# Kernel optimization log

Measured on AMD Instinct MI355X. Metric: run time of the kernel, lower is better.

## Reference

```python
import jax, jax.numpy as jnp
import numpy as np

B, T, D, H = 8, 1024, 1024, 16
HD = D // H  # 64
FF = 4 * D


def setup_inputs() -> dict:
    key = jax.random.key(0)
    ks = jax.random.split(key, 16)
    s = lambda k, shape, scale: (jax.random.normal(k, shape, dtype=jnp.float32) * scale)
    return {
        "x": s(ks[0], (B, T, D), 1.0),
        "ln1_g": jnp.ones((D,), jnp.float32),
        "ln1_b": jnp.zeros((D,), jnp.float32),
        "ln2_g": jnp.ones((D,), jnp.float32),
        "ln2_b": jnp.zeros((D,), jnp.float32),
        "Wq": s(ks[1], (H, D, HD), 0.02), "bq": jnp.zeros((H, HD), jnp.float32),
        "Wk": s(ks[2], (H, D, HD), 0.02), "bk": jnp.zeros((H, HD), jnp.float32),
        "Wv": s(ks[3], (H, D, HD), 0.02), "bv": jnp.zeros((H, HD), jnp.float32),
        "Wo": s(ks[4], (D, D), 0.02), "bo": jnp.zeros((D,), jnp.float32),
        "W1": s(ks[5], (D, FF), 0.02), "b1": jnp.zeros((FF,), jnp.float32),
        "W2": s(ks[6], (FF, D), 0.02), "b2": jnp.zeros((D,), jnp.float32),
    }


def layer_norm(x, g, b, eps=1e-5):
    mu = jnp.mean(x, axis=-1, keepdims=True)
    var = jnp.mean(jnp.square(x - mu), axis=-1, keepdims=True)
    return (x - mu) * jax.lax.rsqrt(var + eps) * g + b


def reference(x, ln1_g, ln1_b, ln2_g, ln2_b, Wq, bq, Wk, bk, Wv, bv, Wo, bo, W1, b1, W2, b2):
    h = layer_norm(x, ln1_g, ln1_b)
    # Per-head Q/K/V projections, batched over heads (equivalent to the
    # Python loop of per-head Linears in the original module).
    q = jnp.einsum("btd,hde->bhte", h, Wq) + bq[None, :, None, :]
    k = jnp.einsum("btd,hde->bhte", h, Wk) + bk[None, :, None, :]
    v = jnp.einsum("btd,hde->bhte", h, Wv) + bv[None, :, None, :]
    scores = jnp.einsum("bhte,bhse->bhts", q, k) / jnp.sqrt(jnp.float32(HD))
    att = jax.nn.softmax(scores, axis=-1)  # no causal mask in source
    ctx = jnp.einsum("bhts,bhse->bhte", att, v)
    # concat heads along feature dim
    ctx = jnp.transpose(ctx, (0, 2, 1, 3)).reshape(B, T, D)
    attn_out = ctx @ Wo + bo
    x = x + attn_out
    h2 = layer_norm(x, ln2_g, ln2_b)
    ff = jax.nn.gelu(h2 @ W1 + b1, approximate=False) @ W2 + b2
    return x + ff
```

## Files before the change

kernel.cpp:

```cpp
#include <hip/hip_runtime.h>
#include <hip/hip_bf16.h>
#include <cstdint>
#include <cstddef>


typedef __bf16 bf16;
typedef __bf16 bf16x8 __attribute__((ext_vector_type(8)));
typedef __bf16 bf16x4 __attribute__((ext_vector_type(4)));
typedef float  f32x4  __attribute__((ext_vector_type(4)));
typedef uint32_t u32x4 __attribute__((ext_vector_type(4)));

#define BB    8
#define TT    1024
#define DD    1024
#define HH    16
#define HDIM  64
#define FFD   4096
#define MROWS (BB*TT)

__device__ __forceinline__ void async_ld16(const void* g, void* l) {
  __builtin_amdgcn_global_load_lds(
      (const __attribute__((address_space(1))) uint32_t*)g,
      (__attribute__((address_space(3))) uint32_t*)l, 16, 0, 0);
}

__device__ __forceinline__ float gelu_f(float v) {
  float z = 0.7978845608028654f * (v + 0.044715f * v * v * v);
  z = fminf(fmaxf(z, -9.0f), 9.0f);
  const float e = __expf(-2.0f * z);
  const float th = 1.0f - __fdividef(2.0f * e, 1.0f + e);
  return 0.5f * v * (1.0f + th);
}

__device__ __forceinline__ float exp2_fast(float x) {
  float r; asm("v_exp_f32 %0, %1" : "=v"(r) : "v"(x)); return r;
}
__device__ __forceinline__ uint32_t cvt_pk_bf16(float a, float b) {
  uint32_t r; asm("v_cvt_pk_bf16_f32 %0, %1, %2" : "=v"(r) : "v"(a), "v"(b));
  return r;
}

__global__ void k_transpose_cast(const float* __restrict__ src, bf16* __restrict__ dst,
                                 int K, int N) {
  __shared__ float tile[32][33];
  const size_t boff = (size_t)blockIdx.z * K * N;
  src += boff; dst += boff;
  const int k0 = blockIdx.y * 32, n0 = blockIdx.x * 32;
  const int tx = threadIdx.x, ty = threadIdx.y;
#pragma unroll
  for (int i = 0; i < 4; ++i)
    tile[ty + i*8][tx] = src[(size_t)(k0 + ty + i*8) * N + n0 + tx];
  __syncthreads();
#pragma unroll
  for (int i = 0; i < 4; ++i)
    dst[(size_t)(n0 + ty + i*8) * K + k0 + tx] = (bf16)tile[tx][ty + i*8];
}

__global__ void k_concat_bias(const float* __restrict__ bq, const float* __restrict__ bk,
                              const float* __restrict__ bv, float* __restrict__ out) {
  int i = blockIdx.x * 256 + threadIdx.x;
  float v = (i < 1024) ? bq[i] : (i < 2048) ? bk[i - 1024] : bv[i - 2048];
  out[i] = v;
}

__global__ void k_transpose_v(const bf16* __restrict__ qkv, bf16* __restrict__ vT) {
  __shared__ bf16 tile[32][33];
  const int bh = blockIdx.z;
  const int b = bh >> 4, h = bh & 15;
  const int t0 = blockIdx.x * 32, e0 = blockIdx.y * 32;
  const int tx = threadIdx.x, ty = threadIdx.y;
  const bf16* src = qkv + (size_t)b * TT * 3072 + 2048 + h * 64;
#pragma unroll
  for (int i = 0; i < 4; ++i)
    tile[ty + i*8][tx] = src[(size_t)(t0 + ty + i*8) * 3072 + e0 + tx];
  __syncthreads();
  bf16* dst = vT + ((size_t)bh * 64 + e0) * TT + t0;
#pragma unroll
  for (int i = 0; i < 4; ++i)
    dst[(size_t)(ty + i*8) * TT + tx] = tile[tx][ty + i*8];
}

__global__ void k_layernorm(const float* __restrict__ x, const float* __restrict__ g,
                            const float* __restrict__ b, bf16* __restrict__ out) {
  const int row = blockIdx.x, tid = threadIdx.x;
  const float* xr = x + (size_t)row * DD;
  f32x4 v = *(const f32x4*)(xr + tid * 4);
  float s  = v[0] + v[1] + v[2] + v[3];
  float ss = v[0]*v[0] + v[1]*v[1] + v[2]*v[2] + v[3]*v[3];
#pragma unroll
  for (int m = 1; m < 64; m <<= 1) { s += __shfl_xor(s, m); ss += __shfl_xor(ss, m); }
  __shared__ float red[8];
  const int wid = tid >> 6;
  if ((tid & 63) == 0) { red[wid*2] = s; red[wid*2+1] = ss; }
  __syncthreads();
  s  = red[0] + red[2] + red[4] + red[6];
  ss = red[1] + red[3] + red[5] + red[7];
  const float mu = s * (1.0f / DD);
  const float var = ss * (1.0f / DD) - mu * mu;
  const float rs = rsqrtf(var + 1e-5f);
  bf16x4 o;
#pragma unroll
  for (int j = 0; j < 4; ++j)
    o[j] = (bf16)((v[j] - mu) * rs * g[tid*4 + j] + b[tid*4 + j]);
  *(bf16x4*)&out[(size_t)row * DD + tid * 4] = o;
}

#define RD_B(reg, base) { _Pragma("unroll") \
    for (int nf = 0; nf < 4; ++nf) reg[nf] = *(const bf16x8*)((base) + nf*1024); }
#define RD_A4(reg, base, mb) { _Pragma("unroll") \
    for (int mf = 0; mf < 4; ++mf) reg[mf] = *(const bf16x8*)((base) + (mb+mf)*1024); }
#define MM(areg, breg, mb) { _Pragma("unroll") \
    for (int mf = 0; mf < 4; ++mf) _Pragma("unroll") \
      for (int nf = 0; nf < 4; ++nf) \
        acc[mb+mf][nf] = __builtin_amdgcn_mfma_f32_16x16x32_bf16(areg[mf], breg[nf], acc[mb+mf][nf], 0, 0, 0); }
#define SGA(off, lb) { async_ld16(aG0 + (off), (lb)+0*64);   async_ld16(aG1 + (off), (lb)+64*64); \
                       async_ld16(aG2 + (off), (lb)+128*64); async_ld16(aG3 + (off), (lb)+192*64); }
#define SGB(off, lb) { async_ld16(bG0 + (off), (lb)+0*64);   async_ld16(bG1 + (off), (lb)+64*64); \
                       async_ld16(bG2 + (off), (lb)+128*64); async_ld16(bG3 + (off), (lb)+192*64); }
#define SGB2a(off, lb) { async_ld16(bG0 + (off), (lb)+0*64);   async_ld16(bG1 + (off), (lb)+64*64); }
#define SGB2b(off, lb) { async_ld16(bG2 + (off), (lb)+128*64); async_ld16(bG3 + (off), (lb)+192*64); }
#define WAIT_LGKM { asm volatile("s_waitcnt lgkmcnt(0)" ::: "memory"); __builtin_amdgcn_sched_barrier(0); }
#define VMC(n)  { asm volatile("s_waitcnt vmcnt(" #n ")" ::: "memory"); __builtin_amdgcn_sched_barrier(0); }
#define BAR __builtin_amdgcn_s_barrier()
#define PR1 __builtin_amdgcn_s_setprio(1)
#define PR0 __builtin_amdgcn_s_setprio(0)

#define GEMM256_PREAMBLE \
  __shared__ __align__(16) bf16 As[2][256 * 64]; \
  __shared__ __align__(16) bf16 Bs[2][256 * 64]; \
  const int tid = threadIdx.x; \
  const int w = tid >> 6, l = tid & 63; \
  const int wm = w >> 2, wn = w & 3; \
  const int l15 = l & 15, l4 = l >> 4; \
  const int nbx = N >> 8; \
  const int nwg = gridDim.x; \
  const int cpx = nwg >> 3; \
  const int swz = (blockIdx.x & 7) * cpx + (blockIdx.x >> 3); \
  const int m0 = (swz / nbx) << 8, n0 = (swz % nbx) << 8; \
  f32x4 acc[8][4] = {}; \
  const int l7 = l15 & 7; \
  const int c0 = (l4 ^ l7) * 8; \
  const int c1 = ((4 + l4) ^ l7) * 8; \
  const bf16* const A00 = &As[0][(wm*128 + l15)*64 + c0]; \
  const bf16* const A01 = &As[0][(wm*128 + l15)*64 + c1]; \
  const bf16* const A10 = &As[1][(wm*128 + l15)*64 + c0]; \
  const bf16* const A11 = &As[1][(wm*128 + l15)*64 + c1]; \
  const bf16* const B00 = &Bs[0][(wn*64 + l15)*64 + c0]; \
  const bf16* const B01 = &Bs[0][(wn*64 + l15)*64 + c1]; \
  const bf16* const B10 = &Bs[1][(wn*64 + l15)*64 + c0]; \
  const bf16* const B11 = &Bs[1][(wn*64 + l15)*64 + c1]; \
  const int srow = l >> 3, sch = l & 7; \
  const int schx = (sch ^ srow) * 8; \
  const bf16* const aG0 = A  + (size_t)(m0 + w*8 + srow) * K + schx; \
  const bf16* const aG1 = aG0 + (size_t)64 * K; \
  const bf16* const aG2 = aG0 + (size_t)128 * K; \
  const bf16* const aG3 = aG0 + (size_t)192 * K; \
  const bf16* const bG0 = Bt + (size_t)(n0 + w*8 + srow) * K + schx; \
  const bf16* const bG1 = bG0 + (size_t)64 * K; \
  const bf16* const bG2 = bG0 + (size_t)128 * K; \
  const bf16* const bG3 = bG0 + (size_t)192 * K; \
  bf16* const LA0 = (bf16*)As[0] + w*512; \
  bf16* const LA1 = (bf16*)As[1] + w*512; \
  bf16* const LB0 = (bf16*)Bs[0] + w*512; \
  bf16* const LB1 = (bf16*)Bs[1] + w*512; \
  const int NT = K >> 6;

#define GEMM256_EPILOGUE \
  _Pragma("unroll") \
  for (int mf = 0; mf < 8; ++mf) { \
    _Pragma("unroll") \
    for (int r = 0; r < 4; ++r) { \
      const size_t grow = (size_t)(m0 + wm*128 + mf*16 + l4*4 + r); \
      const size_t rowoff = grow * (size_t)N; \
      _Pragma("unroll") \
      for (int nf = 0; nf < 4; ++nf) { \
        const int gcol = n0 + wn*64 + nf*16 + l15; \
        float v = acc[mf][nf][r] + bias[gcol]; \
        if constexpr (MODE == 1) v = gelu_f(v); \
        outb[rowoff + gcol] = (bf16)v; \
      } \
    } \
  }

template<int MODE>
__global__ __launch_bounds__(512, 2)
void k_gemm256(const bf16* __restrict__ A, const bf16* __restrict__ Bt,
               const float* __restrict__ bias, bf16* __restrict__ outb,
               int M, int N, int K) {
  GEMM256_PREAMBLE

  SGA(0, LA0)  SGB2a(0, LB0) SGB2b(0, LB0)  SGA(64, LA1)
  VMC(4);
  BAR;

  size_t ko = 0;
  for (int T = 0; T < NT; T += 2) {
    const bool nl  = (T + 2 < NT);
    const bool nl2 = (T + 3 < NT);
    bf16x8 b0[4], b1[4], alo[4], ahi[4];

    RD_B(b0, B00) RD_A4(alo, A00, 0)
    SGB2a(ko + 64, LB1)
    BAR; WAIT_LGKM;
    PR1; MM(alo, b0, 0) PR0;
    BAR;
    RD_A4(ahi, A00, 4)
    SGB2b(ko + 64, LB1)
    BAR; WAIT_LGKM;
    PR1; MM(ahi, b0, 4) PR0;
    BAR;
    RD_B(b1, B01) RD_A4(alo, A01, 0) RD_A4(ahi, A01, 4)
    BAR; WAIT_LGKM;
    PR1; MM(alo, b1, 0) PR0;
    BAR;
    if (nl) SGA(ko + 128, LA0)
    PR1; MM(ahi, b1, 4) PR0;
    if (nl) { VMC(4); } else { VMC(0); }
    BAR;

    RD_B(b0, B10) RD_A4(alo, A10, 0)
    if (nl) SGB2a(ko + 128, LB0)
    BAR; WAIT_LGKM;
    PR1; MM(alo, b0, 0) PR0;
    BAR;
    RD_A4(ahi, A10, 4)
    if (nl) SGB2b(ko + 128, LB0)
    BAR; WAIT_LGKM;
    PR1; MM(ahi, b0, 4) PR0;
    BAR;
    RD_B(b1, B11) RD_A4(alo, A11, 0) RD_A4(ahi, A11, 4)
    BAR; WAIT_LGKM;
    PR1; MM(alo, b1, 0) PR0;
    BAR;
    if (nl2) SGA(ko + 192, LA1)
    PR1; MM(ahi, b1, 4) PR0;
    if (nl2) { VMC(4); } else { VMC(0); }
    BAR;

    ko += 128;
  }

  GEMM256_EPILOGUE
}

template<int MODE>
__global__ __launch_bounds__(512, 2)
void k_gemm256b(const bf16* __restrict__ A, const bf16* __restrict__ Bt,
                const float* __restrict__ bias, bf16* __restrict__ outb,
                int M, int N, int K) {
  GEMM256_PREAMBLE

  SGA(0, LA0)  SGB(0, LB0)  SGA(64, LA1)  SGB(64, LB1)
  VMC(8);
  BAR;

  size_t ko = 0;
  for (int T = 0; T < NT; T += 2) {
    const bool nl  = (T + 2 < NT);
    const bool nl2 = (T + 3 < NT);
    bf16x8 b0[4], b1[4], alo[4], ahi[4];

    RD_B(b0, B00) RD_A4(alo, A00, 0)
    BAR; WAIT_LGKM;
    PR1; MM(alo, b0, 0) PR0;
    BAR;
    RD_A4(ahi, A00, 4)
    BAR; WAIT_LGKM;
    PR1; MM(ahi, b0, 4) PR0;
    BAR;
    RD_B(b1, B01) RD_A4(alo, A01, 0) RD_A4(ahi, A01, 4)
    BAR; WAIT_LGKM;
    PR1; MM(alo, b1, 0) PR0;
    BAR;
    if (nl) { SGA(ko + 128, LA0) SGB(ko + 128, LB0) }
    PR1; MM(ahi, b1, 4) PR0;
    if (nl) { VMC(8); } else { VMC(0); }
    BAR;

    RD_B(b0, B10) RD_A4(alo, A10, 0)
    BAR; WAIT_LGKM;
    PR1; MM(alo, b0, 0) PR0;
    BAR;
    RD_A4(ahi, A10, 4)
    BAR; WAIT_LGKM;
    PR1; MM(ahi, b0, 4) PR0;
    BAR;
    RD_B(b1, B11) RD_A4(alo, A11, 0) RD_A4(ahi, A11, 4)
    BAR; WAIT_LGKM;
    PR1; MM(alo, b1, 0) PR0;
    BAR;
    if (nl2) { SGA(ko + 192, LA1) SGB(ko + 192, LB1) }
    PR1; MM(ahi, b1, 4) PR0;
    if (nl2) { VMC(8); } else { VMC(0); }
    BAR;

    ko += 128;
  }

  GEMM256_EPILOGUE
}

template<int MODE>
__global__ __launch_bounds__(256)
void k_gemm(const bf16* __restrict__ A, const bf16* __restrict__ Bt,
            const float* __restrict__ bias, const float* __restrict__ res,
            bf16* __restrict__ outb, float* __restrict__ outf,
            int M, int N, int K) {
  __shared__ __align__(16) bf16 As[128 * 64];
  __shared__ __align__(16) bf16 Bs[128 * 64];
  const int tid = threadIdx.x;
  const int w = tid >> 6, l = tid & 63;
  const int wm = w >> 1, wn = w & 1;
  const int l15 = l & 15, l4 = l >> 4;
  const int m0 = blockIdx.y * 128, n0 = blockIdx.x * 128;

  f32x4 acc[4][4] = {};

  const int l7 = l15 & 7;
  const int c0 = (l4 ^ l7) * 8, c1 = ((4 + l4) ^ l7) * 8;
  const bf16* const Ab = &As[(wm*64 + l15)*64];
  const bf16* const Bb = &Bs[(wn*64 + l15)*64];

  const int sr8 = l >> 3, sl7 = l & 7;
  const int schx = (sl7 ^ sr8) * 8;
  const bf16* const gA0 = A  + (size_t)(m0 + w*32 + sr8) * K + schx;
  const bf16* const gA1 = gA0 + (size_t)8 * K;
  const bf16* const gA2 = gA0 + (size_t)16 * K;
  const bf16* const gA3 = gA0 + (size_t)24 * K;
  const bf16* const gB0 = Bt + (size_t)(n0 + w*32 + sr8) * K + schx;
  const bf16* const gB1 = gB0 + (size_t)8 * K;
  const bf16* const gB2 = gB0 + (size_t)16 * K;
  const bf16* const gB3 = gB0 + (size_t)24 * K;
  bf16* const lA = (bf16*)As + w*32*64;
  bf16* const lB = (bf16*)Bs + w*32*64;

  for (int k0 = 0; k0 < K; k0 += 64) {
    async_ld16(gA0 + k0, lA);          async_ld16(gA1 + k0, lA + 8*64);
    async_ld16(gA2 + k0, lA + 16*64);  async_ld16(gA3 + k0, lA + 24*64);
    async_ld16(gB0 + k0, lB);          async_ld16(gB1 + k0, lB + 8*64);
    async_ld16(gB2 + k0, lB + 16*64);  async_ld16(gB3 + k0, lB + 24*64);
    __syncthreads();
#pragma unroll
    for (int kk = 0; kk < 2; ++kk) {
      const int cc = kk ? c1 : c0;
      bf16x8 af[4], bfr[4];
#pragma unroll
      for (int mf = 0; mf < 4; ++mf) af[mf] = *(const bf16x8*)(Ab + mf*1024 + cc);
#pragma unroll
      for (int nf = 0; nf < 4; ++nf) bfr[nf] = *(const bf16x8*)(Bb + nf*1024 + cc);
#pragma unroll
      for (int mf = 0; mf < 4; ++mf)
#pragma unroll
        for (int nf = 0; nf < 4; ++nf)
          acc[mf][nf] = __builtin_amdgcn_mfma_f32_16x16x32_bf16(af[mf], bfr[nf], acc[mf][nf], 0, 0, 0);
    }
    __syncthreads();
  }

#pragma unroll
  for (int mf = 0; mf < 4; ++mf) {
#pragma unroll
    for (int r = 0; r < 4; ++r) {
      const size_t grow = (size_t)(m0 + wm*64 + mf*16 + l4*4 + r);
      const size_t rowoff = grow * (size_t)N;
#pragma unroll
      for (int nf = 0; nf < 4; ++nf) {
        const int gcol = n0 + wn*64 + nf*16 + l15;
        float v = acc[mf][nf][r] + bias[gcol];
        if constexpr (MODE == 1) v = gelu_f(v);
        if constexpr (MODE == 2) {
          v += res[rowoff + gcol];
          outf[rowoff + gcol] = v;
        } else {
          outb[rowoff + gcol] = (bf16)v;
        }
      }
    }
  }
}

__global__ __launch_bounds__(512)
void k_attn(const bf16* __restrict__ qkv, const bf16* __restrict__ vT,
            bf16* __restrict__ ctx) {
  const int tid = threadIdx.x;
  const int w = tid >> 6, l = tid & 63;
  const int l15 = l & 15, l4 = l >> 4;

  const int gid = ((int)blockIdx.x & 7) * 128 + ((int)blockIdx.x >> 3);
  const int qt = gid & 7;
  const int bh = gid >> 3;
  const int h = bh & 15, b = bh >> 4;

  __shared__ __align__(16) bf16 Ks[2][64 * 64];
  __shared__ __align__(16) bf16 Vs[2][64 * 64];

  const bf16* base = qkv + (size_t)b * TT * 3072;
  const bf16* Qp = base + h * 64;
  const bf16* Kp = base + 1024 + h * 64;
  const bf16* Vtp = vT + (size_t)bh * HDIM * TT;

  const float SCL = 0.125f * 1.44269504f;
  const float THR = 8.0f * 1.44269504f;

  const int qrow = qt * 128 + w * 16 + l15;
  bf16x8 qf[2];
  {
    bf16x8 q0 = *(const bf16x8*)&Qp[(size_t)qrow * 3072 + l4 * 8];
    bf16x8 q1 = *(const bf16x8*)&Qp[(size_t)qrow * 3072 + 32 + l4 * 8];
#pragma unroll
    for (int j = 0; j < 8; ++j) {
      qf[0][j] = (bf16)((float)q0[j] * SCL);
      qf[1][j] = (bf16)((float)q1[j] * SCL);
    }
  }

  f32x4 oacc[4] = {};
  float mrow = -1e30f;
  float lrow = 0.f;

  const int l7 = l15 & 7;
  const int c0 = (l4 ^ l7) * 8, c1 = ((4 + l4) ^ l7) * 8;

  const int aL0 = (((l4 & 1) << 5) + l15) << 2;
  const int aL1 = aL0 + 64;
  const bool hi = (l & 32) != 0;

  const int srow = w * 8 + (l >> 3);
  const int sch = (l & 7) ^ (srow & 7);

  auto stage = [&](int buf, int t) {
    const int kv0 = t * 64;
    async_ld16(Kp + (size_t)(kv0 + srow) * 3072 + sch * 8, &Ks[buf][w * 512]);
    async_ld16(Vtp + (size_t)srow * TT + kv0 + sch * 8, &Vs[buf][w * 512]);
  };

  stage(0, 0);
  for (int t = 0; t < TT / 64; ++t) {
    const int cur = t & 1;
    __syncthreads();
    if (t + 1 < TT / 64) stage(cur ^ 1, t + 1);

    const bf16* const Kc = &Ks[cur][l15 * 64];
    const bf16* const Vc = &Vs[cur][l15 * 64];

    f32x4 sacc[4] = {};
    __builtin_amdgcn_s_setprio(1);
#pragma unroll
    for (int nf = 0; nf < 4; ++nf) {
      bf16x8 k0 = *(const bf16x8*)(Kc + nf*1024 + c0);
      bf16x8 k1 = *(const bf16x8*)(Kc + nf*1024 + c1);
      sacc[nf] = __builtin_amdgcn_mfma_f32_16x16x32_bf16(k0, qf[0], sacc[nf], 0, 0, 0);
      sacc[nf] = __builtin_amdgcn_mfma_f32_16x16x32_bf16(k1, qf[1], sacc[nf], 0, 0, 0);
    }
    __builtin_amdgcn_s_setprio(0);

    float m = fmaxf(fmaxf(sacc[0][0], sacc[0][1]), fmaxf(sacc[0][2], sacc[0][3]));
#pragma unroll
    for (int nf = 1; nf < 4; ++nf)
      m = fmaxf(m, fmaxf(fmaxf(sacc[nf][0], sacc[nf][1]), fmaxf(sacc[nf][2], sacc[nf][3])));
    m = fmaxf(m, __shfl_xor(m, 16));
    m = fmaxf(m, __shfl_xor(m, 32));

    const int ok = (m <= mrow + THR);
    if (!__all(ok)) {
      const float mn = fmaxf(mrow, m);
      const float e = exp2_fast(mrow - mn);
      mrow = mn;
      lrow *= e;
      const int qb = l4 << 2;
      float e0 = __shfl(e, qb + 0), e1 = __shfl(e, qb + 1);
      float e2 = __shfl(e, qb + 2), e3 = __shfl(e, qb + 3);
#pragma unroll
      for (int nf = 0; nf < 4; ++nf) {
        oacc[nf][0] *= e0; oacc[nf][1] *= e1;
        oacc[nf][2] *= e2; oacc[nf][3] *= e3;
      }
    }

    float p[4][4];
    float ls = 0.f;
    uint32_t pk0[4], pk1[4];
#pragma unroll
    for (int nf = 0; nf < 4; ++nf) {
#pragma unroll
      for (int r = 0; r < 4; ++r) {
        p[nf][r] = exp2_fast(sacc[nf][r] - mrow);
        ls += p[nf][r];
      }
      pk0[nf] = cvt_pk_bf16(p[nf][0], p[nf][1]);
      pk1[nf] = cvt_pk_bf16(p[nf][2], p[nf][3]);
    }
    ls += __shfl_xor(ls, 16);
    ls += __shfl_xor(ls, 32);
    lrow += ls;

    __builtin_amdgcn_s_setprio(1);
#pragma unroll
    for (int kk = 0; kk < 2; ++kk) {
      const int nfa = 2*kk, nfb = 2*kk + 1;
      int u0 = __builtin_amdgcn_ds_bpermute(aL0, (int)pk0[nfa]);
      int u1 = __builtin_amdgcn_ds_bpermute(aL0, (int)pk0[nfb]);
      int v0 = __builtin_amdgcn_ds_bpermute(aL0, (int)pk1[nfa]);
      int v1 = __builtin_amdgcn_ds_bpermute(aL0, (int)pk1[nfb]);
      int x0 = __builtin_amdgcn_ds_bpermute(aL1, (int)pk0[nfa]);
      int x1 = __builtin_amdgcn_ds_bpermute(aL1, (int)pk0[nfb]);
      int y0 = __builtin_amdgcn_ds_bpermute(aL1, (int)pk1[nfa]);
      int y1 = __builtin_amdgcn_ds_bpermute(aL1, (int)pk1[nfb]);
      u32x4 pw;
      pw[0] = (uint32_t)(hi ? u1 : u0);
      pw[1] = (uint32_t)(hi ? v1 : v0);
      pw[2] = (uint32_t)(hi ? x1 : x0);
      pw[3] = (uint32_t)(hi ? y1 : y0);
      bf16x8 pa = __builtin_bit_cast(bf16x8, pw);
      const int cc = kk ? c1 : c0;
#pragma unroll
      for (int nf = 0; nf < 4; ++nf) {
        bf16x8 vb = *(const bf16x8*)(Vc + nf*1024 + cc);
        oacc[nf] = __builtin_amdgcn_mfma_f32_16x16x32_bf16(pa, vb, oacc[nf], 0, 0, 0);
      }
    }
    __builtin_amdgcn_s_setprio(0);
  }

  const int qb = l4 << 2;
  float li0 = 1.0f / __shfl(lrow, qb + 0);
  float li1 = 1.0f / __shfl(lrow, qb + 1);
  float li2 = 1.0f / __shfl(lrow, qb + 2);
  float li3 = 1.0f / __shfl(lrow, qb + 3);
  bf16* outp = ctx + ((size_t)b * TT + qt * 128 + w * 16) * DD + h * 64;
#pragma unroll
  for (int nf = 0; nf < 4; ++nf) {
    outp[(size_t)(qb + 0) * DD + l15 + nf*16] = (bf16)(oacc[nf][0] * li0);
    outp[(size_t)(qb + 1) * DD + l15 + nf*16] = (bf16)(oacc[nf][1] * li1);
    outp[(size_t)(qb + 2) * DD + l15 + nf*16] = (bf16)(oacc[nf][2] * li2);
    outp[(size_t)(qb + 3) * DD + l15 + nf*16] = (bf16)(oacc[nf][3] * li3);
  }
}

extern "C" void kernel_launch(void* const* d_in, const int* in_sizes, int n_in,
                              void* d_out, int out_size, void* d_ws, size_t ws_size,
                              hipStream_t stream) {
  const float* x     = (const float*)d_in[0];
  const float* ln1_g = (const float*)d_in[1];
  const float* ln1_b = (const float*)d_in[2];
  const float* ln2_g = (const float*)d_in[3];
  const float* ln2_b = (const float*)d_in[4];
  const float* Wq    = (const float*)d_in[5];
  const float* bq    = (const float*)d_in[6];
  const float* Wk    = (const float*)d_in[7];
  const float* bk    = (const float*)d_in[8];
  const float* Wv    = (const float*)d_in[9];
  const float* bv    = (const float*)d_in[10];
  const float* Wo    = (const float*)d_in[11];
  const float* bo    = (const float*)d_in[12];
  const float* W1    = (const float*)d_in[13];
  const float* b1    = (const float*)d_in[14];
  const float* W2    = (const float*)d_in[15];
  const float* b2    = (const float*)d_in[16];
  float* out = (float*)d_out;

  char* ws = (char*)d_ws;
  bf16* h1    = (bf16*)(ws + 0);
  bf16* vT    = (bf16*)(ws + 0);
  bf16* qkv   = (bf16*)(ws + 16777216);
  bf16* ctx   = (bf16*)(ws + 67108864);
  bf16* u     = (bf16*)(ws + 16777216);
  float* x1   = (float*)(ws + 83886080);
  bf16* wtqkv = (bf16*)(ws + 117440512);
  bf16* wot   = (bf16*)(ws + 123731968);
  bf16* w1t   = (bf16*)(ws + 125829120);
  bf16* w2t   = (bf16*)(ws + 134217728);
  float* bqkv = (float*)(ws + 142606336);
  bf16* h2 = h1;

  dim3 tb(32, 8);
  k_transpose_cast<<<dim3(2, 32, 16), tb, 0, stream>>>(Wq, wtqkv, DD, HDIM);
  k_transpose_cast<<<dim3(2, 32, 16), tb, 0, stream>>>(Wk, wtqkv + 1024*1024, DD, HDIM);
  k_transpose_cast<<<dim3(2, 32, 16), tb, 0, stream>>>(Wv, wtqkv + 2048*1024, DD, HDIM);
  k_transpose_cast<<<dim3(32, 32, 1), tb, 0, stream>>>(Wo, wot, DD, DD);
  k_transpose_cast<<<dim3(128, 32, 1), tb, 0, stream>>>(W1, w1t, DD, FFD);
  k_transpose_cast<<<dim3(32, 128, 1), tb, 0, stream>>>(W2, w2t, FFD, DD);
  k_concat_bias<<<dim3(12), 256, 0, stream>>>(bq, bk, bv, bqkv);

  k_layernorm<<<dim3(MROWS), 256, 0, stream>>>(x, ln1_g, ln1_b, h1);

  k_gemm256<0><<<dim3((MROWS/256)*(3072/256)), 512, 0, stream>>>(
      h1, wtqkv, bqkv, qkv, MROWS, 3072, DD);

  k_transpose_v<<<dim3(32, 2, 128), tb, 0, stream>>>(qkv, vT);

  k_attn<<<dim3(1024), 512, 0, stream>>>(qkv, vT, ctx);

  k_gemm<2><<<dim3(8, 64), 256, 0, stream>>>(ctx, wot, bo, x,
                                             nullptr, x1, MROWS, DD, DD);

  k_layernorm<<<dim3(MROWS), 256, 0, stream>>>(x1, ln2_g, ln2_b, h2);

  k_gemm256b<1><<<dim3((MROWS/256)*(FFD/256)), 512, 0, stream>>>(
      h2, w1t, b1, u, MROWS, FFD, DD);

  k_gemm<2><<<dim3(8, 64), 256, 0, stream>>>(u, w2t, b2, x1,
                                             nullptr, out, MROWS, DD, FFD);

  (void)in_sizes; (void)n_in; (void)out_size; (void)ws_size;
}
```

Measured before the change: 413.7 us.

## Load FF1 GEMM B operand directly from global into registers, skipping LDS

```diff
diff --git a/kernel.cpp b/kernel.cpp
--- a/kernel.cpp
+++ b/kernel.cpp
@@ -117,53 +117,12 @@
                        async_ld16(aG2 + (off), (lb)+128*64); async_ld16(aG3 + (off), (lb)+192*64); }
 #define SGB(off, lb) { async_ld16(bG0 + (off), (lb)+0*64);   async_ld16(bG1 + (off), (lb)+64*64); \
                        async_ld16(bG2 + (off), (lb)+128*64); async_ld16(bG3 + (off), (lb)+192*64); }
-#define SGB2a(off, lb) { async_ld16(bG0 + (off), (lb)+0*64);   async_ld16(bG1 + (off), (lb)+64*64); }
-#define SGB2b(off, lb) { async_ld16(bG2 + (off), (lb)+128*64); async_ld16(bG3 + (off), (lb)+192*64); }
 #define WAIT_LGKM { asm volatile("s_waitcnt lgkmcnt(0)" ::: "memory"); __builtin_amdgcn_sched_barrier(0); }
+#define LGKM4 { asm volatile("s_waitcnt lgkmcnt(4)" ::: "memory"); __builtin_amdgcn_sched_barrier(0); }
 #define VMC(n)  { asm volatile("s_waitcnt vmcnt(" #n ")" ::: "memory"); __builtin_amdgcn_sched_barrier(0); }
 #define BAR __builtin_amdgcn_s_barrier()
 #define PR1 __builtin_amdgcn_s_setprio(1)
 #define PR0 __builtin_amdgcn_s_setprio(0)
-
-#define GEMM256_PREAMBLE \
-  __shared__ __align__(16) bf16 As[2][256 * 64]; \
-  __shared__ __align__(16) bf16 Bs[2][256 * 64]; \
-  const int tid = threadIdx.x; \
-  const int w = tid >> 6, l = tid & 63; \
-  const int wm = w >> 2, wn = w & 3; \
-  const int l15 = l & 15, l4 = l >> 4; \
-  const int nbx = N >> 8; \
-  const int nwg = gridDim.x; \
-  const int cpx = nwg >> 3; \
-  const int swz = (blockIdx.x & 7) * cpx + (blockIdx.x >> 3); \
-  const int m0 = (swz / nbx) << 8, n0 = (swz % nbx) << 8; \
-  f32x4 acc[8][4] = {}; \
-  const int l7 = l15 & 7; \
-  const int c0 = (l4 ^ l7) * 8; \
-  const int c1 = ((4 + l4) ^ l7) * 8; \
-  const bf16* const A00 = &As[0][(wm*128 + l15)*64 + c0]; \
-  const bf16* const A01 = &As[0][(wm*128 + l15)*64 + c1]; \
-  const bf16* const A10 = &As[1][(wm*128 + l15)*64 + c0]; \
-  const bf16* const A11 = &As[1][(wm*128 + l15)*64 + c1]; \
-  const bf16* const B00 = &Bs[0][(wn*64 + l15)*64 + c0]; \
-  const bf16* const B01 = &Bs[0][(wn*64 + l15)*64 + c1]; \
-  const bf16* const B10 = &Bs[1][(wn*64 + l15)*64 + c0]; \
-  const bf16* const B11 = &Bs[1][(wn*64 + l15)*64 + c1]; \
-  const int srow = l >> 3, sch = l & 7; \
-  const int schx = (sch ^ srow) * 8; \
-  const bf16* const aG0 = A  + (size_t)(m0 + w*8 + srow) * K + schx; \
-  const bf16* const aG1 = aG0 + (size_t)64 * K; \
-  const bf16* const aG2 = aG0 + (size_t)128 * K; \
-  const bf16* const aG3 = aG0 + (size_t)192 * K; \
-  const bf16* const bG0 = Bt + (size_t)(n0 + w*8 + srow) * K + schx; \
-  const bf16* const bG1 = bG0 + (size_t)64 * K; \
-  const bf16* const bG2 = bG0 + (size_t)128 * K; \
-  const bf16* const bG3 = bG0 + (size_t)192 * K; \
-  bf16* const LA0 = (bf16*)As[0] + w*512; \
-  bf16* const LA1 = (bf16*)As[1] + w*512; \
-  bf16* const LB0 = (bf16*)Bs[0] + w*512; \
-  bf16* const LB1 = (bf16*)Bs[1] + w*512; \
-  const int NT = K >> 6;
 
 #define GEMM256_EPILOGUE \
   _Pragma("unroll") \
@@ -184,13 +143,50 @@
 
 template<int MODE>
 __global__ __launch_bounds__(512, 2)
-void k_gemm256(const bf16* __restrict__ A, const bf16* __restrict__ Bt,
-               const float* __restrict__ bias, bf16* __restrict__ outb,
-               int M, int N, int K) {
-  GEMM256_PREAMBLE
-
-  SGA(0, LA0)  SGB2a(0, LB0) SGB2b(0, LB0)  SGA(64, LA1)
-  VMC(4);
+void k_gemm256b(const bf16* __restrict__ A, const bf16* __restrict__ Bt,
+                const float* __restrict__ bias, bf16* __restrict__ outb,
+                int M, int N, int K) {
+  __shared__ __align__(16) bf16 As[2][256 * 64];
+  __shared__ __align__(16) bf16 Bs[2][256 * 64];
+  const int tid = threadIdx.x;
+  const int w = tid >> 6, l = tid & 63;
+  const int wm = w >> 2, wn = w & 3;
+  const int l15 = l & 15, l4 = l >> 4;
+  const int nbx = N >> 8;
+  const int nwg = gridDim.x;
+  const int cpx = nwg >> 3;
+  const int swz = (blockIdx.x & 7) * cpx + (blockIdx.x >> 3);
+  const int m0 = (swz / nbx) << 8, n0 = (swz % nbx) << 8;
+  f32x4 acc[8][4] = {};
+  const int l7 = l15 & 7;
+  const int c0 = (l4 ^ l7) * 8;
+  const int c1 = ((4 + l4) ^ l7) * 8;
+  const bf16* const A00 = &As[0][(wm*128 + l15)*64 + c0];
+  const bf16* const A01 = &As[0][(wm*128 + l15)*64 + c1];
+  const bf16* const A10 = &As[1][(wm*128 + l15)*64 + c0];
+  const bf16* const A11 = &As[1][(wm*128 + l15)*64 + c1];
+  const bf16* const B00 = &Bs[0][(wn*64 + l15)*64 + c0];
+  const bf16* const B01 = &Bs[0][(wn*64 + l15)*64 + c1];
+  const bf16* const B10 = &Bs[1][(wn*64 + l15)*64 + c0];
+  const bf16* const B11 = &Bs[1][(wn*64 + l15)*64 + c1];
+  const int srow = l >> 3, sch = l & 7;
+  const int schx = (sch ^ srow) * 8;
+  const bf16* const aG0 = A  + (size_t)(m0 + w*8 + srow) * K + schx;
+  const bf16* const aG1 = aG0 + (size_t)64 * K;
+  const bf16* const aG2 = aG0 + (size_t)128 * K;
+  const bf16* const aG3 = aG0 + (size_t)192 * K;
+  const bf16* const bG0 = Bt + (size_t)(n0 + w*8 + srow) * K + schx;
+  const bf16* const bG1 = bG0 + (size_t)64 * K;
+  const bf16* const bG2 = bG0 + (size_t)128 * K;
+  const bf16* const bG3 = bG0 + (size_t)192 * K;
+  bf16* const LA0 = (bf16*)As[0] + w*512;
+  bf16* const LA1 = (bf16*)As[1] + w*512;
+  bf16* const LB0 = (bf16*)Bs[0] + w*512;
+  bf16* const LB1 = (bf16*)Bs[1] + w*512;
+  const int NT = K >> 6;
+
+  SGA(0, LA0)  SGB(0, LB0)  SGA(64, LA1)  SGB(64, LB1)
+  VMC(8);
   BAR;
 
   size_t ko = 0;
@@ -200,12 +196,10 @@
     bf16x8 b0[4], b1[4], alo[4], ahi[4];
 
     RD_B(b0, B00) RD_A4(alo, A00, 0)
-    SGB2a(ko + 64, LB1)
     BAR; WAIT_LGKM;
     PR1; MM(alo, b0, 0) PR0;
     BAR;
     RD_A4(ahi, A00, 4)
-    SGB2b(ko + 64, LB1)
     BAR; WAIT_LGKM;
     PR1; MM(ahi, b0, 4) PR0;
     BAR;
@@ -213,18 +207,16 @@
     BAR; WAIT_LGKM;
     PR1; MM(alo, b1, 0) PR0;
     BAR;
-    if (nl) SGA(ko + 128, LA0)
+    if (nl) { SGA(ko + 128, LA0) SGB(ko + 128, LB0) }
     PR1; MM(ahi, b1, 4) PR0;
-    if (nl) { VMC(4); } else { VMC(0); }
+    if (nl) { VMC(8); } else { VMC(0); }
     BAR;
 
     RD_B(b0, B10) RD_A4(alo, A10, 0)
-    if (nl) SGB2a(ko + 128, LB0)
     BAR; WAIT_LGKM;
     PR1; MM(alo, b0, 0) PR0;
     BAR;
     RD_A4(ahi, A10, 4)
-    if (nl) SGB2b(ko + 128, LB0)
     BAR; WAIT_LGKM;
     PR1; MM(ahi, b0, 4) PR0;
     BAR;
@@ -232,9 +224,9 @@
     BAR; WAIT_LGKM;
     PR1; MM(alo, b1, 0) PR0;
     BAR;
-    if (nl2) SGA(ko + 192, LA1)
+    if (nl2) { SGA(ko + 192, LA1) SGB(ko + 192, LB1) }
     PR1; MM(ahi, b1, 4) PR0;
-    if (nl2) { VMC(4); } else { VMC(0); }
+    if (nl2) { VMC(8); } else { VMC(0); }
     BAR;
 
     ko += 128;
@@ -245,57 +237,88 @@
 
 template<int MODE>
 __global__ __launch_bounds__(512, 2)
-void k_gemm256b(const bf16* __restrict__ A, const bf16* __restrict__ Bt,
+void k_gemm256c(const bf16* __restrict__ A, const bf16* __restrict__ Bt,
                 const float* __restrict__ bias, bf16* __restrict__ outb,
                 int M, int N, int K) {
-  GEMM256_PREAMBLE
-
-  SGA(0, LA0)  SGB(0, LB0)  SGA(64, LA1)  SGB(64, LB1)
-  VMC(8);
+  __shared__ __align__(16) bf16 As[2][256 * 64];
+  const int tid = threadIdx.x;
+  const int w = tid >> 6, l = tid & 63;
+  const int wm = w >> 2, wn = w & 3;
+  const int l15 = l & 15, l4 = l >> 4;
+  const int nbx = N >> 8;
+  const int nwg = gridDim.x;
+  const int cpx = nwg >> 3;
+  const int swz = (blockIdx.x & 7) * cpx + (blockIdx.x >> 3);
+  const int m0 = (swz / nbx) << 8, n0 = (swz % nbx) << 8;
+  f32x4 acc[8][4] = {};
+  const int l7 = l15 & 7;
+  const int c0 = (l4 ^ l7) * 8;
+  const int c1 = ((4 + l4) ^ l7) * 8;
+  const bf16* const A00 = &As[0][(wm*128 + l15)*64 + c0];
+  const bf16* const A01 = &As[0][(wm*128 + l15)*64 + c1];
+  const bf16* const A10 = &As[1][(wm*128 + l15)*64 + c0];
+  const bf16* const A11 = &As[1][(wm*128 + l15)*64 + c1];
+  const int srow = l >> 3, sch = l & 7;
+  const int schx = (sch ^ srow) * 8;
+  const bf16* const aG0 = A  + (size_t)(m0 + w*8 + srow) * K + schx;
+  const bf16* const aG1 = aG0 + (size_t)64 * K;
+  const bf16* const aG2 = aG0 + (size_t)128 * K;
+  const bf16* const aG3 = aG0 + (size_t)192 * K;
+  bf16* const LA0 = (bf16*)As[0] + w*512;
+  bf16* const LA1 = (bf16*)As[1] + w*512;
+  const bf16* const bF = Bt + (size_t)(n0 + wn*64 + l15) * K + l4 * 8;
+  const size_t bstride = (size_t)16 * K;
+  const int NT = K >> 6;
+
+#define LDB(reg, off) { _Pragma("unroll") \
+    for (int q = 0; q < 4; ++q) { \
+      reg[q]     = *(const bf16x8*)(bF + (off) + q*bstride); \
+      reg[q + 4] = *(const bf16x8*)(bF + (off) + q*bstride + 32); } }
+
+  bf16x8 bA[8], bB[8];
+
+  LDB(bA, 0)
+  SGA(0, LA0)  SGA(64, LA1)
+  VMC(4);
   BAR;
 
   size_t ko = 0;
   for (int T = 0; T < NT; T += 2) {
     const bool nl  = (T + 2 < NT);
     const bool nl2 = (T + 3 < NT);
-    bf16x8 b0[4], b1[4], alo[4], ahi[4];
-
-    RD_B(b0, B00) RD_A4(alo, A00, 0)
-    BAR; WAIT_LGKM;
-    PR1; MM(alo, b0, 0) PR0;
-    BAR;
-    RD_A4(ahi, A00, 4)
-    BAR; WAIT_LGKM;
-    PR1; MM(ahi, b0, 4) PR0;
-    BAR;
-    RD_B(b1, B01) RD_A4(alo, A01, 0) RD_A4(ahi, A01, 4)
-    BAR; WAIT_LGKM;
-    PR1; MM(alo, b1, 0) PR0;
-    BAR;
-    if (nl) { SGA(ko + 128, LA0) SGB(ko + 128, LB0) }
-    PR1; MM(ahi, b1, 4) PR0;
-    if (nl) { VMC(8); } else { VMC(0); }
-    BAR;
-
-    RD_B(b0, B10) RD_A4(alo, A10, 0)
-    BAR; WAIT_LGKM;
-    PR1; MM(alo, b0, 0) PR0;
-    BAR;
-    RD_A4(ahi, A10, 4)
-    BAR; WAIT_LGKM;
-    PR1; MM(ahi, b0, 4) PR0;
-    BAR;
-    RD_B(b1, B11) RD_A4(alo, A11, 0) RD_A4(ahi, A11, 4)
-    BAR; WAIT_LGKM;
-    PR1; MM(alo, b1, 0) PR0;
-    BAR;
-    if (nl2) { SGA(ko + 192, LA1) SGB(ko + 192, LB1) }
-    PR1; MM(ahi, b1, 4) PR0;
-    if (nl2) { VMC(8); } else { VMC(0); }
+    bf16x8 alo[4], ahi[4];
+
+    RD_A4(alo, A00, 0) RD_A4(ahi, A00, 4)
+    LDB(bB, ko + 64)
+    LGKM4;
+    PR1; MM(alo, bA, 0) PR0;
+    WAIT_LGKM;
+    PR1; MM(ahi, bA, 4) PR0;
+    RD_A4(alo, A01, 0) RD_A4(ahi, A01, 4)
+    WAIT_LGKM;
+    BAR;
+    if (nl) SGA(ko + 128, LA0)
+    PR1; MM(alo, (bA + 4), 0) MM(ahi, (bA + 4), 4) PR0;
+    if (nl) { VMC(4); } else { VMC(0); }
+    BAR;
+
+    RD_A4(alo, A10, 0) RD_A4(ahi, A10, 4)
+    if (nl) LDB(bA, ko + 128)
+    LGKM4;
+    PR1; MM(alo, bB, 0) PR0;
+    WAIT_LGKM;
+    PR1; MM(ahi, bB, 4) PR0;
+    RD_A4(alo, A11, 0) RD_A4(ahi, A11, 4)
+    WAIT_LGKM;
+    BAR;
+    if (nl2) SGA(ko + 192, LA1)
+    PR1; MM(alo, (bB + 4), 0) MM(ahi, (bB + 4), 4) PR0;
+    if (nl2) { VMC(4); } else { VMC(0); }
     BAR;
 
     ko += 128;
   }
+#undef LDB
 
   GEMM256_EPILOGUE
 }
@@ -584,7 +607,7 @@
 
   k_layernorm<<<dim3(MROWS), 256, 0, stream>>>(x, ln1_g, ln1_b, h1);
 
-  k_gemm256<0><<<dim3((MROWS/256)*(3072/256)), 512, 0, stream>>>(
+  k_gemm256b<0><<<dim3((MROWS/256)*(3072/256)), 512, 0, stream>>>(
       h1, wtqkv, bqkv, qkv, MROWS, 3072, DD);
 
   k_transpose_v<<<dim3(32, 2, 128), tb, 0, stream>>>(qkv, vT);
@@ -596,7 +619,7 @@
 
   k_layernorm<<<dim3(MROWS), 256, 0, stream>>>(x1, ln2_g, ln2_b, h2);
 
-  k_gemm256b<1><<<dim3((MROWS/256)*(FFD/256)), 512, 0, stream>>>(
+  k_gemm256c<1><<<dim3((MROWS/256)*(FFD/256)), 512, 0, stream>>>(
       h2, w1t, b1, u, MROWS, FFD, DD);
 
   k_gemm<2><<<dim3(8, 64), 256, 0, stream>>>(u, w2t, b2, x1,
```

Result: slower. 534.9 us (+29.3%).

## Add finer-grained staged-prefetch GEMM for FFN1 and swap QKV to bulk-prefetch GEMM

Applied to the files above, without the earlier changes.

```diff
diff --git a/kernel.cpp b/kernel.cpp
--- a/kernel.cpp
+++ b/kernel.cpp
@@ -117,17 +117,17 @@
                        async_ld16(aG2 + (off), (lb)+128*64); async_ld16(aG3 + (off), (lb)+192*64); }
 #define SGB(off, lb) { async_ld16(bG0 + (off), (lb)+0*64);   async_ld16(bG1 + (off), (lb)+64*64); \
                        async_ld16(bG2 + (off), (lb)+128*64); async_ld16(bG3 + (off), (lb)+192*64); }
-#define SGB2a(off, lb) { async_ld16(bG0 + (off), (lb)+0*64);   async_ld16(bG1 + (off), (lb)+64*64); }
-#define SGB2b(off, lb) { async_ld16(bG2 + (off), (lb)+128*64); async_ld16(bG3 + (off), (lb)+192*64); }
+#define SGA_S0(off, lb) { async_ld16(aG0 + (off), (lb)+0*64);    async_ld16(aG2 + (off), (lb)+128*64); }
+#define SGA_S1(off, lb) { async_ld16(aG1 + (off), (lb)+64*64);   async_ld16(aG3 + (off), (lb)+192*64); }
+#define SGB_Q0(off, lb) { async_ld16(bG0 + (off), (lb)+0*64);    async_ld16(bG1 + (off), (lb)+64*64); }
+#define SGB_Q1(off, lb) { async_ld16(bG2 + (off), (lb)+128*64);  async_ld16(bG3 + (off), (lb)+192*64); }
 #define WAIT_LGKM { asm volatile("s_waitcnt lgkmcnt(0)" ::: "memory"); __builtin_amdgcn_sched_barrier(0); }
 #define VMC(n)  { asm volatile("s_waitcnt vmcnt(" #n ")" ::: "memory"); __builtin_amdgcn_sched_barrier(0); }
 #define BAR __builtin_amdgcn_s_barrier()
 #define PR1 __builtin_amdgcn_s_setprio(1)
 #define PR0 __builtin_amdgcn_s_setprio(0)
 
-#define GEMM256_PREAMBLE \
-  __shared__ __align__(16) bf16 As[2][256 * 64]; \
-  __shared__ __align__(16) bf16 Bs[2][256 * 64]; \
+#define GEMM256_DECLS \
   const int tid = threadIdx.x; \
   const int w = tid >> 6, l = tid & 63; \
   const int wm = w >> 2, wn = w & 3; \
@@ -184,13 +184,15 @@
 
 template<int MODE>
 __global__ __launch_bounds__(512, 2)
-void k_gemm256(const bf16* __restrict__ A, const bf16* __restrict__ Bt,
-               const float* __restrict__ bias, bf16* __restrict__ outb,
-               int M, int N, int K) {
-  GEMM256_PREAMBLE
-
-  SGA(0, LA0)  SGB2a(0, LB0) SGB2b(0, LB0)  SGA(64, LA1)
-  VMC(4);
+void k_gemm256b(const bf16* __restrict__ A, const bf16* __restrict__ Bt,
+                const float* __restrict__ bias, bf16* __restrict__ outb,
+                int M, int N, int K) {
+  __shared__ __align__(16) bf16 As[2][256 * 64];
+  __shared__ __align__(16) bf16 Bs[2][256 * 64];
+  GEMM256_DECLS
+
+  SGA(0, LA0)  SGB(0, LB0)  SGA(64, LA1)  SGB(64, LB1)
+  VMC(8);
   BAR;
 
   size_t ko = 0;
@@ -200,67 +202,6 @@
     bf16x8 b0[4], b1[4], alo[4], ahi[4];
 
     RD_B(b0, B00) RD_A4(alo, A00, 0)
-    SGB2a(ko + 64, LB1)
-    BAR; WAIT_LGKM;
-    PR1; MM(alo, b0, 0) PR0;
-    BAR;
-    RD_A4(ahi, A00, 4)
-    SGB2b(ko + 64, LB1)
-    BAR; WAIT_LGKM;
-    PR1; MM(ahi, b0, 4) PR0;
-    BAR;
-    RD_B(b1, B01) RD_A4(alo, A01, 0) RD_A4(ahi, A01, 4)
-    BAR; WAIT_LGKM;
-    PR1; MM(alo, b1, 0) PR0;
-    BAR;
-    if (nl) SGA(ko + 128, LA0)
-    PR1; MM(ahi, b1, 4) PR0;
-    if (nl) { VMC(4); } else { VMC(0); }
-    BAR;
-
-    RD_B(b0, B10) RD_A4(alo, A10, 0)
-    if (nl) SGB2a(ko + 128, LB0)
-    BAR; WAIT_LGKM;
-    PR1; MM(alo, b0, 0) PR0;
-    BAR;
-    RD_A4(ahi, A10, 4)
-    if (nl) SGB2b(ko + 128, LB0)
-    BAR; WAIT_LGKM;
-    PR1; MM(ahi, b0, 4) PR0;
-    BAR;
-    RD_B(b1, B11) RD_A4(alo, A11, 0) RD_A4(ahi, A11, 4)
-    BAR; WAIT_LGKM;
-    PR1; MM(alo, b1, 0) PR0;
-    BAR;
-    if (nl2) SGA(ko + 192, LA1)
-    PR1; MM(ahi, b1, 4) PR0;
-    if (nl2) { VMC(4); } else { VMC(0); }
-    BAR;
-
-    ko += 128;
-  }
-
-  GEMM256_EPILOGUE
-}
-
-template<int MODE>
-__global__ __launch_bounds__(512, 2)
-void k_gemm256b(const bf16* __restrict__ A, const bf16* __restrict__ Bt,
-                const float* __restrict__ bias, bf16* __restrict__ outb,
-                int M, int N, int K) {
-  GEMM256_PREAMBLE
-
-  SGA(0, LA0)  SGB(0, LB0)  SGA(64, LA1)  SGB(64, LB1)
-  VMC(8);
-  BAR;
-
-  size_t ko = 0;
-  for (int T = 0; T < NT; T += 2) {
-    const bool nl  = (T + 2 < NT);
-    const bool nl2 = (T + 3 < NT);
-    bf16x8 b0[4], b1[4], alo[4], ahi[4];
-
-    RD_B(b0, B00) RD_A4(alo, A00, 0)
     BAR; WAIT_LGKM;
     PR1; MM(alo, b0, 0) PR0;
     BAR;
@@ -292,6 +233,77 @@
     if (nl2) { SGA(ko + 192, LA1) SGB(ko + 192, LB1) }
     PR1; MM(ahi, b1, 4) PR0;
     if (nl2) { VMC(8); } else { VMC(0); }
+    BAR;
+
+    ko += 128;
+  }
+
+  GEMM256_EPILOGUE
+}
+
+template<int MODE>
+__global__ __launch_bounds__(512, 2)
+void k_gemm256p(const bf16* __restrict__ A, const bf16* __restrict__ Bt,
+                const float* __restrict__ bias, bf16* __restrict__ outb,
+                int M, int N, int K) {
+  __shared__ __align__(16) bf16 As[2][256 * 64];
+  __shared__ __align__(16) bf16 Bs[2][256 * 64];
+  GEMM256_DECLS
+
+  SGA_S0(0, LA0) SGA_S1(0, LA0)
+  SGB_Q0(0, LB0) SGB_Q1(0, LB0)
+  SGA_S0(64, LA1)
+  VMC(2);
+  BAR;
+
+  size_t ko = 0;
+  for (int T = 0; T < NT; T += 2) {
+    const bool s2 = (T + 2 < NT);
+    const bool s3 = (T + 3 < NT);
+    bf16x8 b0[4], b1[4], a[4];
+
+    RD_B(b0, B00) RD_A4(a, A00, 0)
+    SGA_S1(ko + 64, LA1)
+    BAR; WAIT_LGKM;
+    PR1; MM(a, b0, 0) PR0;
+    BAR;
+    RD_B(b1, B01) RD_A4(a, A01, 0)
+    SGB_Q0(ko + 64, LB1)
+    BAR; WAIT_LGKM;
+    PR1; MM(a, b1, 0) PR0;
+    BAR;
+    RD_A4(a, A00, 4)
+    SGB_Q1(ko + 64, LB1)
+    BAR; WAIT_LGKM;
+    PR1; MM(a, b0, 4) PR0;
+    BAR;
+    RD_A4(a, A01, 4)
+    if (s2) SGA_S0(ko + 128, LA0)
+    BAR; WAIT_LGKM;
+    PR1; MM(a, b1, 4) PR0;
+    if (s2) { VMC(2); } else { VMC(0); }
+    BAR;
+
+    RD_B(b0, B10) RD_A4(a, A10, 0)
+    if (s2) SGA_S1(ko + 128, LA0)
+    BAR; WAIT_LGKM;
+    PR1; MM(a, b0, 0) PR0;
+    BAR;
+    RD_B(b1, B11) RD_A4(a, A11, 0)
+    if (s2) SGB_Q0(ko + 128, LB0)
+    BAR; WAIT_LGKM;
+    PR1; MM(a, b1, 0) PR0;
+    BAR;
+    RD_A4(a, A10, 4)
+    if (s2) SGB_Q1(ko + 128, LB0)
+    BAR; WAIT_LGKM;
+    PR1; MM(a, b0, 4) PR0;
+    BAR;
+    RD_A4(a, A11, 4)
+    if (s3) SGA_S0(ko + 192, LA1)
+    BAR; WAIT_LGKM;
+    PR1; MM(a, b1, 4) PR0;
+    if (s3) { VMC(2); } else { VMC(0); }
     BAR;
 
     ko += 128;
@@ -584,7 +596,7 @@
 
   k_layernorm<<<dim3(MROWS), 256, 0, stream>>>(x, ln1_g, ln1_b, h1);
 
-  k_gemm256<0><<<dim3((MROWS/256)*(3072/256)), 512, 0, stream>>>(
+  k_gemm256b<0><<<dim3((MROWS/256)*(3072/256)), 512, 0, stream>>>(
       h1, wtqkv, bqkv, qkv, MROWS, 3072, DD);
 
   k_transpose_v<<<dim3(32, 2, 128), tb, 0, stream>>>(qkv, vT);
@@ -596,7 +608,7 @@
 
   k_layernorm<<<dim3(MROWS), 256, 0, stream>>>(x1, ln2_g, ln2_b, h2);
 
-  k_gemm256b<1><<<dim3((MROWS/256)*(FFD/256)), 512, 0, stream>>>(
+  k_gemm256p<1><<<dim3((MROWS/256)*(FFD/256)), 512, 0, stream>>>(
       h2, w1t, b1, u, MROWS, FFD, DD);
 
   k_gemm<2><<<dim3(8, 64), 256, 0, stream>>>(u, w2t, b2, x1,
```

Result: no change. 411.6 us (-0.5%).
